# Kernel optimization log

Measured on AMD Instinct MI355X. Metric: run time of the kernel, lower is better.

Reference implementation:

```python
import jax, jax.numpy as jnp
import numpy as np

EPS = 1e-5

def _layer_norm(x, w, b):
    mu = jnp.mean(x, axis=-1, keepdims=True)
    var = jnp.mean((x - mu) ** 2, axis=-1, keepdims=True)
    return (x - mu) * jax.lax.rsqrt(var + EPS) * w + b

B, N, C, D = 8, 16384, 256, 2
K = 4096  # ceil(N / 4)

def setup_inputs() -> dict:
    key = jax.random.key(0)
    k0, k1, k2, k3 = jax.random.split(key, 4)
    pos = jax.random.uniform(k0, (B, N, D), dtype=jnp.float32)
    feat = jax.random.normal(k1, (B, N, C), dtype=jnp.float32)
    assignment = jax.random.randint(k2, (B, N), 0, K)
    norm_w = jnp.ones((C + D,), jnp.float32)
    norm_b = jnp.zeros((C + D,), jnp.float32)
    lin_w = jax.random.normal(k3, (2 * C, C + D), jnp.float32) * 0.02
    return {"pos": pos, "feat": feat, "assignment": assignment,
            "norm_w": norm_w, "norm_b": norm_b, "lin_w": lin_w}

def reference(pos, feat, assignment, norm_w, norm_b, lin_w):
    b, n, c = feat.shape
    d = pos.shape[2]
    k = K
    # normalize coordinates by per-dim global max
    pos = pos / jnp.max(pos.reshape(-1, d), axis=0)
    # flatten (batch, cluster) into segments for one big segment_sum
    seg = (assignment + jnp.arange(b, dtype=assignment.dtype)[:, None] * k).reshape(-1)  # [b*n]
    count = jax.ops.segment_sum(jnp.ones((b * n,), pos.dtype), seg,
                                num_segments=b * k).reshape(b, k)
    safe = jnp.maximum(count, 1.0)
    # cluster mean position (scatter_add + divide)
    mean_pos = jax.ops.segment_sum(pos.reshape(-1, d), seg,
                                   num_segments=b * k).reshape(b, k, d) / safe[..., None]
    # relative position via gather
    idx = jnp.broadcast_to(assignment[:, :, None], (b, n, d))
    rel_pos = pos - jnp.take_along_axis(mean_pos, idx, axis=1)
    # norm + linear (dim+pos_dim -> 2*dim, no bias)
    h = _layer_norm(jnp.concatenate([feat, rel_pos], axis=-1), norm_w, norm_b)
    h = jnp.einsum('bnf,of->bno', h, lin_w)  # [b, n, 2c]
    # cluster mean pooling of features (segment sum / count)
    merged = jax.ops.segment_sum(h.reshape(b * n, 2 * c), seg,
                                 num_segments=b * k).reshape(b, k, 2 * c) / safe[..., None]
    # zero out empty clusters and emit validity mask (valid_row_idx path)
    valid = (count > 0).astype(merged.dtype)  # [b, k]
    new_feat = merged * valid[..., None]
    new_pos = mean_pos * valid[..., None]
    new_mask = valid[..., None]  # [b, k, 1]
    return (new_pos, new_feat, new_mask)
```

## Files before the change

### kernel.cpp

```cpp
#include <hip/hip_runtime.h>

#define BB 8
#define NN 16384
#define CC 256
#define KK 4096
#define FDIM 258
#define FP 256
#define OC 512
#define NPTS (BB * NN)
#define NROWS (BB * KK)
#define CAP 64
#define LNEPS 1e-5f

#define OUT_FEAT_OFF 65536
#define OUT_MASK_OFF (65536 + 16777216)

#define OFF_MAX 0
#define OFF_ICOUNT 16
#define MEMSET_FLOATS (16 + NROWS)
#define OFF_ACCH 32784
#define ACC_FSLOTS (NROWS * FP / 2)
#define OFF_INV (OFF_ACCH + ACC_FSLOTS)
#define OFF_LIST (OFF_INV + NROWS)
#define OFF_WPH (OFF_LIST + NROWS * CAP)
#define OFF_RP (OFF_WPH + OC * FP / 2)
#define OFF_WC (OFF_RP + NROWS * 2)

typedef _Float16 h8v __attribute__((ext_vector_type(8)));
typedef _Float16 h4v __attribute__((ext_vector_type(4)));
typedef float f4v __attribute__((ext_vector_type(4)));

#define PREP_PB 512
#define PREP_WB 129

__global__ __launch_bounds__(256) void k_prep(const float* __restrict__ pos,
                                              const int* __restrict__ asg,
                                              const float* __restrict__ lw,
                                              float* ws) {
    int bid = blockIdx.x;
    if (bid < PREP_PB) {
        int i = bid * 256 + threadIdx.x;
        int* icount = (int*)(ws + OFF_ICOUNT);
        int* list = (int*)(ws + OFF_LIST);
        float2 p = ((const float2*)pos)[i];
        int b = i >> 14;
        int row = b * KK + asg[i];
        int slot = atomicAdd(icount + row, 1);
        if (slot < CAP) list[row * CAP + slot] = i;
        float mx = p.x, my = p.y;
        for (int off = 32; off > 0; off >>= 1) {
            mx = fmaxf(mx, __shfl_down(mx, off));
            my = fmaxf(my, __shfl_down(my, off));
        }
        if ((threadIdx.x & 63) == 0) {
            atomicMax((int*)(ws + OFF_MAX + 0), __float_as_int(mx));
            atomicMax((int*)(ws + OFF_MAX + 1), __float_as_int(my));
        }
    } else if (bid < PREP_PB + 128) {
        _Float16* Wh = (_Float16*)(ws + OFF_WPH);
        int e = (bid - PREP_PB) * 1024 + threadIdx.x * 4;
        int o = e >> 8, f = e & 255;
        h4v h;
#pragma unroll
        for (int u = 0; u < 4; ++u) h[u] = (_Float16)lw[o * FDIM + f + u];
        *(h4v*)(Wh + e) = h;
    } else {
        int o = threadIdx.x;
        ws[OFF_WC + o] = lw[o * FDIM + 256];
        ws[OFF_WC + 512 + o] = lw[o * FDIM + 257];
        o += 256;
        ws[OFF_WC + o] = lw[o * FDIM + 256];
        ws[OFF_WC + 512 + o] = lw[o * FDIM + 257];
    }
}

__global__ __launch_bounds__(256) void k_gather(
    const float* __restrict__ feat, const float* __restrict__ pos,
    const float* __restrict__ nw, const float* __restrict__ nb,
    float* ws, float* __restrict__ out) {
    int t = threadIdx.x;
    int lane = t & 63;
    int bswz = ((blockIdx.x & 7) << 10) + (blockIdx.x >> 3);
    int row = (bswz << 2) + (t >> 6);
    int q = lane >> 4;
    int ll = lane & 15;
    const int* icount = (const int*)(ws + OFF_ICOUNT);
    const int* list = (const int*)(ws + OFF_LIST);
    _Float16* Ah = (_Float16*)(ws + OFF_ACCH);

    int cnt = icount[row];
    if (cnt > CAP) cnt = CAP;
    float fcnt = (float)cnt;
    float invc = 1.f / fmaxf(fcnt, 1.f);
    float mxx = ws[OFF_MAX + 0], mxy = ws[OFF_MAX + 1];

    int ptl = (lane < cnt) ? list[row * CAP + lane] : 0;
    float px = 0.f, py = 0.f;
    if (lane < cnt) {
        float2 p = ((const float2*)pos)[ptl];
        px = p.x / mxx;
        py = p.y / mxy;
    }
    float sx = px, sy = py;
    for (int m = 32; m; m >>= 1) {
        sx += __shfl_xor(sx, m);
        sy += __shfl_xor(sy, m);
    }
    float meanx = sx * invc, meany = sy * invc;
    float valid = (cnt > 0) ? 1.f : 0.f;
    if (lane == 0) {
        out[2 * row + 0] = meanx * valid;
        out[2 * row + 1] = meany * valid;
        out[OUT_MASK_OFF + row] = valid;
        ws[OFF_INV + row] = invc;
    }

    float4 a0 = {0.f, 0.f, 0.f, 0.f}, a1 = {0.f, 0.f, 0.f, 0.f};
    float4 a2 = {0.f, 0.f, 0.f, 0.f}, a3 = {0.f, 0.f, 0.f, 0.f};
    float arx = 0.f, ary = 0.f;
    for (int s0 = 0; s0 < cnt; s0 += 4) {
        int s = s0 + q;
        int pt = __shfl(ptl, s);
        float rx = __shfl(px, s) - meanx;
        float ry = __shfl(py, s) - meany;
        const float4* fr = (const float4*)(feat + (size_t)pt * CC);
        float4 v0 = fr[ll];
        float4 v1 = fr[16 + ll];
        float4 v2 = fr[32 + ll];
        float4 v3 = fr[48 + ll];
        float S = (v0.x + v0.y + v0.z + v0.w) + (v1.x + v1.y + v1.z + v1.w) +
                  (v2.x + v2.y + v2.z + v2.w) + (v3.x + v3.y + v3.z + v3.w);
        float Q = v0.x * v0.x + v0.y * v0.y + v0.z * v0.z + v0.w * v0.w +
                  v1.x * v1.x + v1.y * v1.y + v1.z * v1.z + v1.w * v1.w +
                  v2.x * v2.x + v2.y * v2.y + v2.z * v2.z + v2.w * v2.w +
                  v3.x * v3.x + v3.y * v3.y + v3.z * v3.z + v3.w * v3.w;
        for (int m = 1; m < 16; m <<= 1) {
            S += __shfl_xor(S, m);
            Q += __shfl_xor(Q, m);
        }
        S += rx + ry;
        Q += rx * rx + ry * ry;
        float mu = S * (1.f / FDIM);
        float var = Q * (1.f / FDIM) - mu * mu;
        float w = (s < cnt) ? rsqrtf(var + LNEPS) : 0.f;
        a0.x += (v0.x - mu) * w; a0.y += (v0.y - mu) * w;
        a0.z += (v0.z - mu) * w; a0.w += (v0.w - mu) * w;
        a1.x += (v1.x - mu) * w; a1.y += (v1.y - mu) * w;
        a1.z += (v1.z - mu) * w; a1.w += (v1.w - mu) * w;
        a2.x += (v2.x - mu) * w; a2.y += (v2.y - mu) * w;
        a2.z += (v2.z - mu) * w; a2.w += (v2.w - mu) * w;
        a3.x += (v3.x - mu) * w; a3.y += (v3.y - mu) * w;
        a3.z += (v3.z - mu) * w; a3.w += (v3.w - mu) * w;
        arx += (rx - mu) * w;
        ary += (ry - mu) * w;
    }
#define MRG(x)              \
    x += __shfl_xor(x, 16); \
    x += __shfl_xor(x, 32);
    MRG(a0.x) MRG(a0.y) MRG(a0.z) MRG(a0.w)
    MRG(a1.x) MRG(a1.y) MRG(a1.z) MRG(a1.w)
    MRG(a2.x) MRG(a2.y) MRG(a2.z) MRG(a2.w)
    MRG(a3.x) MRG(a3.y) MRG(a3.z) MRG(a3.w)
    MRG(arx) MRG(ary)
#undef MRG

    float4 w4 = ((const float4*)nw)[lane];
    float4 b4 = ((const float4*)nb)[lane];
    float4 aq = (q == 0) ? a0 : (q == 1) ? a1 : (q == 2) ? a2 : a3;
    h4v h;
    h[0] = (_Float16)(aq.x * w4.x + fcnt * b4.x);
    h[1] = (_Float16)(aq.y * w4.y + fcnt * b4.y);
    h[2] = (_Float16)(aq.z * w4.z + fcnt * b4.z);
    h[3] = (_Float16)(aq.w * w4.w + fcnt * b4.w);
    *(h4v*)(Ah + (size_t)row * FP + lane * 4) = h;
    if (lane == 0) {
        ws[OFF_RP + 2 * row + 0] = arx * nw[256] + fcnt * nb[256];
        ws[OFF_RP + 2 * row + 1] = ary * nw[257] + fcnt * nb[257];
    }
}

#define GM 128
#define GN 128
#define GK 64

__global__ __launch_bounds__(256) void k_gemm(const float* __restrict__ ws,
                                              float* __restrict__ out) {
    __shared__ __align__(16) _Float16 As[GM * GK];
    __shared__ __align__(16) _Float16 Bs[GN * GK];
    const _Float16* Ah = (const _Float16*)(ws + OFF_ACCH);
    const _Float16* Wh = (const _Float16*)(ws + OFF_WPH);
    const float* inv = ws + OFF_INV;
    const float* rp = ws + OFF_RP;

    int t = threadIdx.x;
    int lane = t & 63;
    int wv = t >> 6;
    int wr = wv & 1, wc = wv >> 1;
    int wg = blockIdx.x;
    int idx = wg >> 3;
    int rowtile = ((wg & 7) << 5) + (idx >> 2);
    int row0 = rowtile * GM;
    int col0 = (idx & 3) * GN;
    int l15 = lane & 15, kq = lane >> 4;
    int sw = l15 & 7;

    f4v acc[4][4] = {};

    for (int k0 = 0; k0 < FP; k0 += GK) {
#pragma unroll
        for (int l = 0; l < 4; ++l) {
            int c = l * 256 + t;
            int r = c >> 3;
            int ch = (c & 7) ^ (r & 7);
            int lb = (l * 256 + wv * 64) * 8;
            __builtin_amdgcn_global_load_lds(
                (const __attribute__((address_space(1))) void*)(
                    Ah + (size_t)(row0 + r) * FP + k0 + ch * 8),
                (__attribute__((address_space(3))) void*)(As + lb), 16, 0, 0);
            __builtin_amdgcn_global_load_lds(
                (const __attribute__((address_space(1))) void*)(
                    Wh + (size_t)(col0 + r) * FP + k0 + ch * 8),
                (__attribute__((address_space(3))) void*)(Bs + lb), 16, 0, 0);
        }
        __syncthreads();
#pragma unroll
        for (int ks = 0; ks < 2; ++ks) {
            h8v af[4], bf[4];
            int lc = ((ks << 2) | kq);
#pragma unroll
            for (int i = 0; i < 4; ++i)
                af[i] = *(const h8v*)&As[(wr * 64 + i * 16 + l15) * GK + ((lc ^ sw) * 8)];
#pragma unroll
            for (int j = 0; j < 4; ++j)
                bf[j] = *(const h8v*)&Bs[(wc * 64 + j * 16 + l15) * GK + ((lc ^ sw) * 8)];
#pragma unroll
            for (int i = 0; i < 4; ++i)
#pragma unroll
                for (int j = 0; j < 4; ++j)
                    acc[i][j] = __builtin_amdgcn_mfma_f32_16x16x32_f16(
                        af[i], bf[j], acc[i][j], 0, 0, 0);
        }
        __syncthreads();
    }

    float w0[4], w1[4];
#pragma unroll
    for (int j = 0; j < 4; ++j) {
        int col = col0 + wc * 64 + j * 16 + l15;
        w0[j] = ws[OFF_WC + col];
        w1[j] = ws[OFF_WC + 512 + col];
    }
#pragma unroll
    for (int i = 0; i < 4; ++i) {
#pragma unroll
        for (int r = 0; r < 4; ++r) {
            int row = row0 + wr * 64 + i * 16 + kq * 4 + r;
            float sc = inv[row];
            float r0 = rp[2 * row], r1 = rp[2 * row + 1];
#pragma unroll
            for (int j = 0; j < 4; ++j) {
                int col = col0 + wc * 64 + j * 16 + l15;
                out[OUT_FEAT_OFF + (size_t)row * OC + col] =
                    (acc[i][j][r] + r0 * w0[j] + r1 * w1[j]) * sc;
            }
        }
    }
}

extern "C" void kernel_launch(void* const* d_in, const int* in_sizes, int n_in,
                              void* d_out, int out_size, void* d_ws, size_t ws_size,
                              hipStream_t stream) {
    const float* pos = (const float*)d_in[0];
    const float* feat = (const float*)d_in[1];
    const int* asg = (const int*)d_in[2];
    const float* nw = (const float*)d_in[3];
    const float* nb = (const float*)d_in[4];
    const float* lw = (const float*)d_in[5];
    float* out = (float*)d_out;
    float* ws = (float*)d_ws;

    hipMemsetAsync(d_ws, 0, (size_t)MEMSET_FLOATS * sizeof(float), stream);
    k_prep<<<PREP_PB + PREP_WB, 256, 0, stream>>>(pos, asg, lw, ws);
    k_gather<<<NROWS / 4, 256, 0, stream>>>(feat, pos, nw, nb, ws, out);
    k_gemm<<<NROWS / GM * (OC / GN), 256, 0, stream>>>(ws, out);
}
```

Measured before the change: 303.1 us.

## Double-buffer GEMM LDS tiles with K-step 32 to overlap loads and MFMA

```diff
diff --git a/kernel.cpp b/kernel.cpp
--- a/kernel.cpp
+++ b/kernel.cpp
@@ -181,12 +181,12 @@
 
 #define GM 128
 #define GN 128
-#define GK 64
+#define GK2 32
 
 __global__ __launch_bounds__(256) void k_gemm(const float* __restrict__ ws,
                                               float* __restrict__ out) {
-    __shared__ __align__(16) _Float16 As[GM * GK];
-    __shared__ __align__(16) _Float16 Bs[GN * GK];
+    __shared__ __align__(16) _Float16 As[2][GM * GK2];
+    __shared__ __align__(16) _Float16 Bs[2][GN * GK2];
     const _Float16* Ah = (const _Float16*)(ws + OFF_ACCH);
     const _Float16* Wh = (const _Float16*)(ws + OFF_WPH);
     const float* inv = ws + OFF_INV;
@@ -202,46 +202,66 @@
     int row0 = rowtile * GM;
     int col0 = (idx & 3) * GN;
     int l15 = lane & 15, kq = lane >> 4;
-    int sw = l15 & 7;
+    int sw2 = (l15 >> 1) & 3;
+
+    int c0 = t, c1 = 256 + t;
+    int r0s = c0 >> 2, r1s = c1 >> 2;
+    int ch0 = (c0 & 3) ^ ((r0s >> 1) & 3);
+    int ch1 = (c1 & 3) ^ ((r1s >> 1) & 3);
+    int lb0 = (wv * 64) * 8;
+    int lb1 = (256 + wv * 64) * 8;
+    const _Float16* gA0 = Ah + (size_t)(row0 + r0s) * FP + ch0 * 8;
+    const _Float16* gA1 = Ah + (size_t)(row0 + r1s) * FP + ch1 * 8;
+    const _Float16* gB0 = Wh + (size_t)(col0 + r0s) * FP + ch0 * 8;
+    const _Float16* gB1 = Wh + (size_t)(col0 + r1s) * FP + ch1 * 8;
+
+#define STAGE(buf, k0)                                                        \
+    do {                                                                      \
+        __builtin_amdgcn_global_load_lds(                                     \
+            (const __attribute__((address_space(1))) void*)(gA0 + (k0)),      \
+            (__attribute__((address_space(3))) void*)(&As[buf][0] + lb0), 16, \
+            0, 0);                                                            \
+        __builtin_amdgcn_global_load_lds(                                     \
+            (const __attribute__((address_space(1))) void*)(gA1 + (k0)),      \
+            (__attribute__((address_space(3))) void*)(&As[buf][0] + lb1), 16, \
+            0, 0);                                                            \
+        __builtin_amdgcn_global_load_lds(                                     \
+            (const __attribute__((address_space(1))) void*)(gB0 + (k0)),      \
+            (__attribute__((address_space(3))) void*)(&Bs[buf][0] + lb0), 16, \
+            0, 0);                                                            \
+        __builtin_amdgcn_global_load_lds(                                     \
+            (const __attribute__((address_space(1))) void*)(gB1 + (k0)),      \
+            (__attribute__((address_space(3))) void*)(&Bs[buf][0] + lb1), 16, \
+            0, 0);                                                            \
+    } while (0)
 
     f4v acc[4][4] = {};
 
-    for (int k0 = 0; k0 < FP; k0 += GK) {
-#pragma unroll
-        for (int l = 0; l < 4; ++l) {
-            int c = l * 256 + t;
-            int r = c >> 3;
-            int ch = (c & 7) ^ (r & 7);
-            int lb = (l * 256 + wv * 64) * 8;
-            __builtin_amdgcn_global_load_lds(
-                (const __attribute__((address_space(1))) void*)(
-                    Ah + (size_t)(row0 + r) * FP + k0 + ch * 8),
-                (__attribute__((address_space(3))) void*)(As + lb), 16, 0, 0);
-            __builtin_amdgcn_global_load_lds(
-                (const __attribute__((address_space(1))) void*)(
-                    Wh + (size_t)(col0 + r) * FP + k0 + ch * 8),
-                (__attribute__((address_space(3))) void*)(Bs + lb), 16, 0, 0);
-        }
+    STAGE(0, 0);
+    __syncthreads();
+
+    int cur = 0;
+#pragma unroll
+    for (int tstep = 0; tstep < 8; ++tstep) {
+        if (tstep < 7) STAGE(cur ^ 1, (tstep + 1) * GK2);
+        h8v af[4], bf[4];
+        int lc = kq ^ sw2;
+#pragma unroll
+        for (int i = 0; i < 4; ++i)
+            af[i] = *(const h8v*)&As[cur][(wr * 64 + i * 16 + l15) * GK2 + lc * 8];
+#pragma unroll
+        for (int j = 0; j < 4; ++j)
+            bf[j] = *(const h8v*)&Bs[cur][(wc * 64 + j * 16 + l15) * GK2 + lc * 8];
+#pragma unroll
+        for (int i = 0; i < 4; ++i)
+#pragma unroll
+            for (int j = 0; j < 4; ++j)
+                acc[i][j] = __builtin_amdgcn_mfma_f32_16x16x32_f16(
+                    af[i], bf[j], acc[i][j], 0, 0, 0);
         __syncthreads();
-#pragma unroll
-        for (int ks = 0; ks < 2; ++ks) {
-            h8v af[4], bf[4];
-            int lc = ((ks << 2) | kq);
-#pragma unroll
-            for (int i = 0; i < 4; ++i)
-                af[i] = *(const h8v*)&As[(wr * 64 + i * 16 + l15) * GK + ((lc ^ sw) * 8)];
-#pragma unroll
-            for (int j = 0; j < 4; ++j)
-                bf[j] = *(const h8v*)&Bs[(wc * 64 + j * 16 + l15) * GK + ((lc ^ sw) * 8)];
-#pragma unroll
-            for (int i = 0; i < 4; ++i)
-#pragma unroll
-                for (int j = 0; j < 4; ++j)
-                    acc[i][j] = __builtin_amdgcn_mfma_f32_16x16x32_f16(
-                        af[i], bf[j], acc[i][j], 0, 0, 0);
-        }
-        __syncthreads();
-    }
+        cur ^= 1;
+    }
+#undef STAGE
 
     float w0[4], w1[4];
 #pragma unroll
```

Result: no change. 308.6 us (+1.8%).
